# Kernel tuning notes

Measured on AMD Instinct MI355X. Metric: run time of the kernel, lower is better.

The kernel has to match this reference:

```python
import jax, jax.numpy as jnp
import numpy as np
from jax import lax

B, H, W = 32, 40, 256
FREQ = 40            # freq_num
WIND = 0.5           # wind_size (seconds)
KF = 5               # input_filter_kernel (odd -> 'same' length)
CNN_OUT = 64 * 36 * 252  # out_channels[-1] * (H-4) * (W-4)


def setup_inputs() -> dict:
    key = jax.random.key(0)
    ks = jax.random.split(key, 9)
    return {
        "inputs": jax.random.normal(ks[0], (B, 1, H, W), jnp.float32),
        "w0": jax.random.normal(ks[1], (32, 1, 3, 3), jnp.float32) * 0.1,
        "b0": jax.random.normal(ks[2], (32,), jnp.float32) * 0.05,
        "w1": jax.random.normal(ks[3], (64, 32, 3, 3), jnp.float32) * 0.05,
        "b1": jax.random.normal(ks[4], (64,), jnp.float32) * 0.05,
        "wf": jax.random.normal(ks[5], (1, 1, 1, KF), jnp.float32) * 0.2,
        "bf": jax.random.normal(ks[6], (1,), jnp.float32) * 0.05,
        "wr": jax.random.normal(ks[7], (FREQ, CNN_OUT), jnp.float32) * 1e-3,
        "br": jax.random.normal(ks[8], (FREQ,), jnp.float32) * 0.05,
    }


def _conv2d(x, w, padding):
    return lax.conv_general_dilated(
        x, w, window_strides=(1, 1), padding=padding,
        dimension_numbers=("NCHW", "OIHW", "NCHW"))


def reference(inputs, w0, b0, w1, b1, wf, bf, wr, br):
    b, _, h, w_len = inputs.shape
    # input_filter: Conv1d(1,1,KF, padding=KF//2) applied independently per
    # frequency row -> equivalent to a 2D conv with a (1,KF) kernel.
    p = KF // 2
    feats = _conv2d(inputs, wf, [(0, 0), (p, p)]) + bf[None, :, None, None]  # [B,1,H,W]

    # conv stack with ReLU
    x = jax.nn.relu(_conv2d(inputs, w0, "VALID") + b0[None, :, None, None])
    x = jax.nn.relu(_conv2d(x, w1, "VALID") + b1[None, :, None, None])

    gates = jax.nn.sigmoid(x.reshape(b, -1) @ wr.T + br)

    fs = (1.0 / WIND) * jnp.linspace(1.0, FREQ, FREQ)          # [FREQ]
    wtd_mean_mod = jnp.mean(gates * fs[None, :])               # scalar

    # Fused modulation transform: instead of the per-frequency python loop
    # with materialized [B,H,W] broadcasts, compute sin/cos bases [FREQ,W]
    # and reduce over time with a single einsum each.
    t = jnp.linspace(0.0, WIND, w_len)                          # [W]
    phase = (2.0 * np.pi) * fs[:, None] * t[None, :]            # [FREQ,W]
    f0 = feats[:, 0]                                            # [B,H,W]
    inv_w = jnp.float32(1.0 / w_len)
    sins = jnp.einsum("fw,bhw->bfh", jnp.sin(phase), f0) * inv_w  # mean over W
    coss = jnp.einsum("fw,bhw->bfh", jnp.cos(phase), f0) * inv_w
    mag = jnp.sqrt(sins * sins + coss * coss)                   # [B,FREQ,H]
    mods = (mag * gates[:, :, None]).reshape(b, FREQ * h)       # cat over freq, dim=1
    return mods, wtd_mean_mod
```

## Files before the change

kernel.cpp:

```cpp
#include <hip/hip_runtime.h>
#include <hip/hip_bf16.h>
#include <math.h>

#define BB   32
#define HH   40
#define WW   256
#define NF   40
#define H1N  36
#define W1N  252
#define KCNN 580608
#define KPW  192

typedef __attribute__((ext_vector_type(8))) short bf16x8;
typedef __attribute__((ext_vector_type(4))) float f32x4;

static __device__ __forceinline__ unsigned short f2bf(float v) {
    __hip_bfloat16 h = __float2bfloat16(v);
    return *(unsigned short*)&h;
}

static __device__ __forceinline__ bf16x8 packbf(float4 lo, float4 hi) {
    bf16x8 r;
    r[0] = (short)f2bf(lo.x); r[1] = (short)f2bf(lo.y);
    r[2] = (short)f2bf(lo.z); r[3] = (short)f2bf(lo.w);
    r[4] = (short)f2bf(hi.x); r[5] = (short)f2bf(hi.y);
    r[6] = (short)f2bf(hi.z); r[7] = (short)f2bf(hi.w);
    return r;
}

__global__ void k0_prep_w1(const float* __restrict__ w1, unsigned short* __restrict__ w1c,
                           float* __restrict__ gacc, float* __restrict__ out) {
    int o = blockIdx.x * 256 + threadIdx.x;
    int c0  = o & 31;
    int c1  = (o >> 5) & 63;
    int tap = o >> 11;
    w1c[o] = f2bf(w1[(c1 * 32 + c0) * 9 + tap]);
    if (blockIdx.x == 0) {
        for (int p = threadIdx.x; p < 1280; p += 256) gacc[p] = 0.0f;
        if (threadIdx.x == 0) out[51200] = 0.0f;
    }
}

__global__ __launch_bounds__(256) void k1_conv(
        const float* __restrict__ inp, const float* __restrict__ w0,
        const float* __restrict__ b0, const unsigned short* __restrict__ w1c,
        const float* __restrict__ b1, unsigned short* __restrict__ xbf) {
    __shared__ __align__(16) char smem[33856];
    float* ins = (float*)smem;
    unsigned short* y0T = (unsigned short*)(smem + 2176);
    unsigned short* stg = (unsigned short*)smem;

    const int jt = blockIdx.x;
    const int it = blockIdx.y;
    const int b  = blockIdx.z;
    const int i0 = it * 4;
    const int j0 = jt * 64;
    const int tid = threadIdx.x;

    for (int s = tid; s < 544; s += 256) {
        int r = s / 68, c = s - r * 68;
        int gc = j0 + c;
        ins[s] = (gc < WW) ? inp[(b * HH + i0 + r) * WW + gc] : 0.0f;
    }
    __syncthreads();

    {
        const int c0 = tid & 31;
        const int pg = tid >> 5;
        float wreg[9];
        #pragma unroll
        for (int k = 0; k < 9; ++k) wreg[k] = w0[c0 * 9 + k];
        const float bias = b0[c0];
        for (int it2 = 0; it2 < 50; ++it2) {
            int pos = it2 * 8 + pg;
            if (pos < 396) {
                int r   = pos / 66;
                int col = pos - r * 66;
                float v = 0.0f;
                if (j0 + col < 254) {
                    float a = bias;
                    #pragma unroll
                    for (int ki = 0; ki < 3; ++ki)
                        #pragma unroll
                        for (int kj = 0; kj < 3; ++kj)
                            a = fmaf(ins[(r + ki) * 68 + col + kj], wreg[ki * 3 + kj], a);
                    v = fmaxf(a, 0.0f);
                }
                y0T[pos * 40 + c0] = f2bf(v);
            }
        }
    }
    __syncthreads();

    const int w    = tid >> 6;
    const int lane = tid & 63;
    const int l15  = lane & 15;
    const int quad = lane >> 4;

    float biasr[4][4];
    #pragma unroll
    for (int mt = 0; mt < 4; ++mt)
        #pragma unroll
        for (int rg = 0; rg < 4; ++rg)
            biasr[mt][rg] = b1[mt * 16 + quad * 4 + rg];

    f32x4 acc[4][4];
    #pragma unroll
    for (int mt = 0; mt < 4; ++mt)
        #pragma unroll
        for (int nt = 0; nt < 4; ++nt)
            acc[mt][nt] = (f32x4){0.f, 0.f, 0.f, 0.f};

    #pragma unroll
    for (int ki = 0; ki < 3; ++ki) {
        #pragma unroll
        for (int kj = 0; kj < 3; ++kj) {
            const int tap = ki * 3 + kj;
            bf16x8 af[4], bfr[4];
            #pragma unroll
            for (int mt = 0; mt < 4; ++mt)
                af[mt] = *(const bf16x8*)(w1c + ((tap * 64 + mt * 16 + l15) * 32 + quad * 8));
            #pragma unroll
            for (int nt = 0; nt < 4; ++nt)
                bfr[nt] = *(const bf16x8*)(y0T + (((w + ki) * 66 + nt * 16 + l15 + kj) * 40 + quad * 8));
            #pragma unroll
            for (int mt = 0; mt < 4; ++mt)
                #pragma unroll
                for (int nt = 0; nt < 4; ++nt)
                    acc[mt][nt] = __builtin_amdgcn_mfma_f32_16x16x32_bf16(
                        af[mt], bfr[nt], acc[mt][nt], 0, 0, 0);
        }
    }

    __syncthreads();
    #pragma unroll
    for (int mt = 0; mt < 4; ++mt)
        #pragma unroll
        for (int nt = 0; nt < 4; ++nt)
            #pragma unroll
            for (int rg = 0; rg < 4; ++rg) {
                int c1 = mt * 16 + quad * 4 + rg;
                int j  = nt * 16 + l15;
                int jr = (j + (((c1 >> 2) & 3) << 4)) & 63;
                float v = fmaxf(acc[mt][nt][rg] + biasr[mt][rg], 0.0f);
                stg[(c1 * 4 + w) * 64 + jr] = f2bf(v);
            }
    __syncthreads();

    const int limit = (j0 + 64 <= W1N) ? 64 : (W1N - j0);
    for (int it2 = 0; it2 < 16; ++it2) {
        int cc = it2 * 256 + tid;
        int e  = cc * 4;
        int c1 = e >> 8;
        int w2 = (e >> 6) & 3;
        int jb = e & 63;
        if (jb < limit) {
            int jr = (jb + (((c1 >> 2) & 3) << 4)) & 63;
            *(uint2*)(xbf + (size_t)b * KCNN + (c1 * H1N + i0 + w2) * W1N + j0 + jb) =
                *(const uint2*)(stg + (c1 * 4 + w2) * 64 + jr);
        }
    }
}

__global__ __launch_bounds__(256) void k2_gemm(
        const unsigned short* __restrict__ xbf, const float* __restrict__ wr,
        float* __restrict__ gacc) {
    __shared__ float red[4][32][41];

    const int tid  = threadIdx.x;
    const int wv   = tid >> 6;
    const int lane = tid & 63;
    const int l15  = lane & 15;
    const int quad = lane >> 4;
    const size_t kw = (size_t)(blockIdx.x * 4 + wv) * KPW;

    const unsigned short* ap0 = xbf + (size_t)l15 * KCNN + kw + quad * 8;
    const unsigned short* ap1 = ap0 + (size_t)16 * KCNN;
    const float* bp0 = wr + (size_t)l15 * KCNN + kw + quad * 8;
    const float* bp1 = bp0 + (size_t)16 * KCNN;
    const bool v2 = (l15 < 8);
    const float* bp2 = bp0 + (size_t)32 * KCNN;

    f32x4 acc[2][3];
    #pragma unroll
    for (int mt = 0; mt < 2; ++mt)
        #pragma unroll
        for (int nt = 0; nt < 3; ++nt)
            acc[mt][nt] = (f32x4){0.f, 0.f, 0.f, 0.f};

    const float4 fz = {0.f, 0.f, 0.f, 0.f};
    bf16x8 a0c, a1c, a0n, a1n;
    float4 bw[3][2], bwn[3][2];

    a0c = *(const bf16x8*)ap0;
    a1c = *(const bf16x8*)ap1;
    bw[0][0] = *(const float4*)bp0; bw[0][1] = *(const float4*)(bp0 + 4);
    bw[1][0] = *(const float4*)bp1; bw[1][1] = *(const float4*)(bp1 + 4);
    if (v2) { bw[2][0] = *(const float4*)bp2; bw[2][1] = *(const float4*)(bp2 + 4); }
    else    { bw[2][0] = fz; bw[2][1] = fz; }

    for (int c = 0; c < 6; ++c) {
        if (c < 5) {
            const int o2 = (c + 1) * 32;
            a0n = *(const bf16x8*)(ap0 + o2);
            a1n = *(const bf16x8*)(ap1 + o2);
            bwn[0][0] = *(const float4*)(bp0 + o2); bwn[0][1] = *(const float4*)(bp0 + o2 + 4);
            bwn[1][0] = *(const float4*)(bp1 + o2); bwn[1][1] = *(const float4*)(bp1 + o2 + 4);
            if (v2) { bwn[2][0] = *(const float4*)(bp2 + o2); bwn[2][1] = *(const float4*)(bp2 + o2 + 4); }
            else    { bwn[2][0] = fz; bwn[2][1] = fz; }
        }
        #pragma unroll
        for (int nt = 0; nt < 3; ++nt) {
            bf16x8 bfrag = packbf(bw[nt][0], bw[nt][1]);
            acc[0][nt] = __builtin_amdgcn_mfma_f32_16x16x32_bf16(a0c, bfrag, acc[0][nt], 0, 0, 0);
            acc[1][nt] = __builtin_amdgcn_mfma_f32_16x16x32_bf16(a1c, bfrag, acc[1][nt], 0, 0, 0);
        }
        if (c < 5) {
            a0c = a0n; a1c = a1n;
            #pragma unroll
            for (int nt = 0; nt < 3; ++nt) { bw[nt][0] = bwn[nt][0]; bw[nt][1] = bwn[nt][1]; }
        }
    }

    #pragma unroll
    for (int mt = 0; mt < 2; ++mt)
        #pragma unroll
        for (int nt = 0; nt < 3; ++nt)
            #pragma unroll
            for (int rg = 0; rg < 4; ++rg) {
                int bb = mt * 16 + quad * 4 + rg;
                int ff = nt * 16 + l15;
                if (ff < NF) red[wv][bb][ff] = acc[mt][nt][rg];
            }
    __syncthreads();
    for (int p = tid; p < 1280; p += 256) {
        int bb = p / 40, ff = p - bb * 40;
        float s = 0.0f;
        #pragma unroll
        for (int w = 0; w < 4; ++w) s += red[w][bb][ff];
        atomicAdd(gacc + p, s);
    }
}

__global__ void k3_gates(const float* __restrict__ gacc, const float* __restrict__ br,
                         float* __restrict__ gates, float* __restrict__ out) {
    int p = blockIdx.x * 64 + threadIdx.x;
    int f = p % 40;
    float g = 1.0f / (1.0f + __expf(-(gacc[p] + br[f])));
    gates[p] = g;
    float c = g * (2.0f * (float)(f + 1)) * (1.0f / 1280.0f);
    #pragma unroll
    for (int off = 32; off >= 1; off >>= 1)
        c += __shfl_down(c, off, 64);
    if (threadIdx.x == 0) atomicAdd(out + 51200, c);
}

__global__ __launch_bounds__(320) void k4_mods(
        const float* __restrict__ inp, const float* __restrict__ wf,
        const float* __restrict__ bfp, const float* __restrict__ gates,
        float* __restrict__ out) {
    const int f = blockIdx.x, b = blockIdx.y;
    const int tid = threadIdx.x;
    const int h  = tid >> 3;
    const int wl = tid & 7;
    float wfv[5];
    #pragma unroll
    for (int t = 0; t < 5; ++t) wfv[t] = wf[t];
    const float bias = bfp[0];
    const float cph = 6.283185307179586f * (float)(f + 1) / 255.0f;
    const float* row = inp + (b * HH + h) * WW;
    float sa = 0.0f, ca = 0.0f;
    for (int m = 0; m < 32; ++m) {
        int w = wl + 8 * m;
        float feat = bias;
        #pragma unroll
        for (int d = -2; d <= 2; ++d) {
            int wc = w + d;
            if (wc >= 0 && wc < WW) feat = fmaf(row[wc], wfv[d + 2], feat);
        }
        float sv, cv;
        __sincosf(cph * (float)w, &sv, &cv);
        sa = fmaf(sv, feat, sa);
        ca = fmaf(cv, feat, ca);
    }
    #pragma unroll
    for (int off = 4; off >= 1; off >>= 1) {
        sa += __shfl_xor(sa, off, 8);
        ca += __shfl_xor(ca, off, 8);
    }
    if (wl == 0) {
        float mag = sqrtf(sa * sa + ca * ca) * (1.0f / 256.0f);
        out[b * 1600 + f * 40 + h] = mag * gates[b * 40 + f];
    }
}

extern "C" void kernel_launch(void* const* d_in, const int* in_sizes, int n_in,
                              void* d_out, int out_size, void* d_ws, size_t ws_size,
                              hipStream_t stream) {
    const float* inp = (const float*)d_in[0];
    const float* w0  = (const float*)d_in[1];
    const float* b0  = (const float*)d_in[2];
    const float* w1  = (const float*)d_in[3];
    const float* b1  = (const float*)d_in[4];
    const float* wf  = (const float*)d_in[5];
    const float* bf_ = (const float*)d_in[6];
    const float* wr  = (const float*)d_in[7];
    const float* br  = (const float*)d_in[8];
    float* out = (float*)d_out;

    char* ws = (char*)d_ws;
    unsigned short* xbf = (unsigned short*)ws;
    unsigned short* w1c = (unsigned short*)(ws + 37158912);
    float* gacc  = (float*)(ws + 37195776);
    float* gates = (float*)(ws + 37200896);

    k0_prep_w1<<<72, 256, 0, stream>>>(w1, w1c, gacc, out);
    k1_conv<<<dim3(4, 9, 32), 256, 0, stream>>>(inp, w0, b0, w1c, b1, xbf);
    k2_gemm<<<756, 256, 0, stream>>>(xbf, wr, gacc);
    k3_gates<<<20, 64, 0, stream>>>(gacc, br, gates, out);
    k4_mods<<<dim3(40, 32), 320, 0, stream>>>(inp, wf, bf_, gates, out);
}
```

Baseline: 225.8 us.

## Fuse gates into GEMM tail, tabulate sin/cos, register-block conv0, spread atomics

Several changes land together. The gates kernel is folded into the tail of the regression GEMM through a last-block counter, and the GEMM's atomic accumulation is spread across 8 replica buffers to cut contention. The sin/cos bases are precomputed into tables in the prep kernel and read by the modulation kernel. The first conv layer is restructured so each of 6 thread groups handles one output row using float4 register windows, replacing the strided per-position loop. Together these aim to remove a launch, reduce atomic serialization and trig cost, and cut LDS reads in conv0, at the cost of extra workspace and a threadfence/counter pattern.

```diff
diff --git a/kernel.cpp b/kernel.cpp
--- a/kernel.cpp
+++ b/kernel.cpp
@@ -10,6 +10,7 @@
 #define W1N  252
 #define KCNN 580608
 #define KPW  192
+#define NBLK2 756
 
 typedef __attribute__((ext_vector_type(8))) short bf16x8;
 typedef __attribute__((ext_vector_type(4))) float f32x4;
@@ -28,17 +29,23 @@
     return r;
 }
 
-__global__ void k0_prep_w1(const float* __restrict__ w1, unsigned short* __restrict__ w1c,
-                           float* __restrict__ gacc, float* __restrict__ out) {
+__global__ void k0_prep(const float* __restrict__ w1, unsigned short* __restrict__ w1c,
+                        float* __restrict__ gacc8, float* __restrict__ sintab,
+                        float* __restrict__ costab, float* __restrict__ out,
+                        int* __restrict__ cnt) {
     int o = blockIdx.x * 256 + threadIdx.x;
     int c0  = o & 31;
     int c1  = (o >> 5) & 63;
     int tap = o >> 11;
     w1c[o] = f2bf(w1[(c1 * 32 + c0) * 9 + tap]);
-    if (blockIdx.x == 0) {
-        for (int p = threadIdx.x; p < 1280; p += 256) gacc[p] = 0.0f;
-        if (threadIdx.x == 0) out[51200] = 0.0f;
-    }
+    if (o < 10240) {
+        int f = o >> 8, w = o & 255;
+        float ph = 6.283185307179586f * (float)(f + 1) * (1.0f / 255.0f) * (float)w;
+        sintab[o] = sinf(ph);
+        costab[o] = cosf(ph);
+        gacc8[o] = 0.0f;
+    }
+    if (o == 0) { out[51200] = 0.0f; cnt[0] = 0; }
 }
 
 __global__ __launch_bounds__(256) void k1_conv(
@@ -67,26 +74,56 @@
     {
         const int c0 = tid & 31;
         const int pg = tid >> 5;
-        float wreg[9];
-        #pragma unroll
-        for (int k = 0; k < 9; ++k) wreg[k] = w0[c0 * 9 + k];
-        const float bias = b0[c0];
-        for (int it2 = 0; it2 < 50; ++it2) {
-            int pos = it2 * 8 + pg;
-            if (pos < 396) {
-                int r   = pos / 66;
-                int col = pos - r * 66;
-                float v = 0.0f;
-                if (j0 + col < 254) {
+        if (pg < 6) {
+            float wreg[9];
+            #pragma unroll
+            for (int k = 0; k < 9; ++k) wreg[k] = w0[c0 * 9 + k];
+            const float bias = b0[c0];
+            const float4* rp0 = (const float4*)(ins + (pg    ) * 68);
+            const float4* rp1 = (const float4*)(ins + (pg + 1) * 68);
+            const float4* rp2 = (const float4*)(ins + (pg + 2) * 68);
+            unsigned short* yrow = y0T + pg * 66 * 40 + c0;
+            float4 a0 = rp0[0], a1 = rp1[0], a2 = rp2[0];
+            #pragma unroll 2
+            for (int ch = 0; ch < 8; ++ch) {
+                float4 b0v = rp0[2 * ch + 1], c0v = rp0[2 * ch + 2];
+                float4 b1v = rp1[2 * ch + 1], c1v = rp1[2 * ch + 2];
+                float4 b2v = rp2[2 * ch + 1], c2v = rp2[2 * ch + 2];
+                float r0[12] = {a0.x,a0.y,a0.z,a0.w,b0v.x,b0v.y,b0v.z,b0v.w,c0v.x,c0v.y,c0v.z,c0v.w};
+                float r1[12] = {a1.x,a1.y,a1.z,a1.w,b1v.x,b1v.y,b1v.z,b1v.w,c1v.x,c1v.y,c1v.z,c1v.w};
+                float r2[12] = {a2.x,a2.y,a2.z,a2.w,b2v.x,b2v.y,b2v.z,b2v.w,c2v.x,c2v.y,c2v.z,c2v.w};
+                #pragma unroll
+                for (int t = 0; t < 8; ++t) {
+                    int col = ch * 8 + t;
                     float a = bias;
                     #pragma unroll
-                    for (int ki = 0; ki < 3; ++ki)
-                        #pragma unroll
-                        for (int kj = 0; kj < 3; ++kj)
-                            a = fmaf(ins[(r + ki) * 68 + col + kj], wreg[ki * 3 + kj], a);
-                    v = fmaxf(a, 0.0f);
+                    for (int kj = 0; kj < 3; ++kj) {
+                        a = fmaf(r0[t + kj], wreg[kj],     a);
+                        a = fmaf(r1[t + kj], wreg[3 + kj], a);
+                        a = fmaf(r2[t + kj], wreg[6 + kj], a);
+                    }
+                    float v = (j0 + col < 254) ? fmaxf(a, 0.0f) : 0.0f;
+                    yrow[col * 40] = f2bf(v);
                 }
-                y0T[pos * 40 + c0] = f2bf(v);
+                a0 = c0v; a1 = c1v; a2 = c2v;
+            }
+            {
+                float t0[4] = {a0.x, a0.y, a0.z, a0.w};
+                float t1[4] = {a1.x, a1.y, a1.z, a1.w};
+                float t2[4] = {a2.x, a2.y, a2.z, a2.w};
+                #pragma unroll
+                for (int t = 0; t < 2; ++t) {
+                    int col = 64 + t;
+                    float a = bias;
+                    #pragma unroll
+                    for (int kj = 0; kj < 3; ++kj) {
+                        a = fmaf(t0[t + kj], wreg[kj],     a);
+                        a = fmaf(t1[t + kj], wreg[3 + kj], a);
+                        a = fmaf(t2[t + kj], wreg[6 + kj], a);
+                    }
+                    float v = (j0 + col < 254) ? fmaxf(a, 0.0f) : 0.0f;
+                    yrow[col * 40] = f2bf(v);
+                }
             }
         }
     }
@@ -164,8 +201,11 @@
 
 __global__ __launch_bounds__(256) void k2_gemm(
         const unsigned short* __restrict__ xbf, const float* __restrict__ wr,
-        float* __restrict__ gacc) {
+        float* __restrict__ gacc8, const float* __restrict__ br,
+        float* __restrict__ gates, float* __restrict__ out, int* __restrict__ cnt) {
     __shared__ float red[4][32][41];
+    __shared__ float wsum[4];
+    __shared__ int lastflag;
 
     const int tid  = threadIdx.x;
     const int wv   = tid >> 6;
@@ -233,30 +273,42 @@
                 if (ff < NF) red[wv][bb][ff] = acc[mt][nt][rg];
             }
     __syncthreads();
+    float* myg = gacc8 + (size_t)(blockIdx.x & 7) * 1280;
     for (int p = tid; p < 1280; p += 256) {
         int bb = p / 40, ff = p - bb * 40;
         float s = 0.0f;
         #pragma unroll
         for (int w = 0; w < 4; ++w) s += red[w][bb][ff];
-        atomicAdd(gacc + p, s);
-    }
-}
-
-__global__ void k3_gates(const float* __restrict__ gacc, const float* __restrict__ br,
-                         float* __restrict__ gates, float* __restrict__ out) {
-    int p = blockIdx.x * 64 + threadIdx.x;
-    int f = p % 40;
-    float g = 1.0f / (1.0f + __expf(-(gacc[p] + br[f])));
-    gates[p] = g;
-    float c = g * (2.0f * (float)(f + 1)) * (1.0f / 1280.0f);
-    #pragma unroll
-    for (int off = 32; off >= 1; off >>= 1)
-        c += __shfl_down(c, off, 64);
-    if (threadIdx.x == 0) atomicAdd(out + 51200, c);
+        atomicAdd(myg + p, s);
+    }
+
+    __threadfence();
+    __syncthreads();
+    if (tid == 0) lastflag = (atomicAdd(cnt, 1) == NBLK2 - 1) ? 1 : 0;
+    __syncthreads();
+    if (lastflag) {
+        float c = 0.0f;
+        for (int p = tid; p < 1280; p += 256) {
+            float s = 0.0f;
+            #pragma unroll
+            for (int r = 0; r < 8; ++r)
+                s += atomicAdd(gacc8 + r * 1280 + p, 0.0f);
+            int f = p % 40;
+            float g = 1.0f / (1.0f + __expf(-(s + br[f])));
+            gates[p] = g;
+            c += g * (2.0f * (float)(f + 1)) * (1.0f / 1280.0f);
+        }
+        #pragma unroll
+        for (int off = 32; off >= 1; off >>= 1) c += __shfl_down(c, off, 64);
+        if ((tid & 63) == 0) wsum[tid >> 6] = c;
+        __syncthreads();
+        if (tid == 0) out[51200] = wsum[0] + wsum[1] + wsum[2] + wsum[3];
+    }
 }
 
 __global__ __launch_bounds__(320) void k4_mods(
-        const float* __restrict__ inp, const float* __restrict__ wf,
+        const float* __restrict__ inp, const float* __restrict__ sintab,
+        const float* __restrict__ costab, const float* __restrict__ wf,
         const float* __restrict__ bfp, const float* __restrict__ gates,
         float* __restrict__ out) {
     const int f = blockIdx.x, b = blockIdx.y;
@@ -267,8 +319,9 @@
     #pragma unroll
     for (int t = 0; t < 5; ++t) wfv[t] = wf[t];
     const float bias = bfp[0];
-    const float cph = 6.283185307179586f * (float)(f + 1) / 255.0f;
-    const float* row = inp + (b * HH + h) * WW;
+    const float* row  = inp + (b * HH + h) * WW;
+    const float* srow = sintab + f * 256;
+    const float* crow = costab + f * 256;
     float sa = 0.0f, ca = 0.0f;
     for (int m = 0; m < 32; ++m) {
         int w = wl + 8 * m;
@@ -278,10 +331,8 @@
             int wc = w + d;
             if (wc >= 0 && wc < WW) feat = fmaf(row[wc], wfv[d + 2], feat);
         }
-        float sv, cv;
-        __sincosf(cph * (float)w, &sv, &cv);
-        sa = fmaf(sv, feat, sa);
-        ca = fmaf(cv, feat, ca);
+        sa = fmaf(srow[w], feat, sa);
+        ca = fmaf(crow[w], feat, ca);
     }
     #pragma unroll
     for (int off = 4; off >= 1; off >>= 1) {
@@ -311,12 +362,14 @@
     char* ws = (char*)d_ws;
     unsigned short* xbf = (unsigned short*)ws;
     unsigned short* w1c = (unsigned short*)(ws + 37158912);
-    float* gacc  = (float*)(ws + 37195776);
-    float* gates = (float*)(ws + 37200896);
-
-    k0_prep_w1<<<72, 256, 0, stream>>>(w1, w1c, gacc, out);
+    float* gacc8  = (float*)(ws + 37195776);
+    float* gates  = (float*)(ws + 37236736);
+    float* sintab = (float*)(ws + 37241856);
+    float* costab = (float*)(ws + 37282816);
+    int*   cnt    = (int*)(ws + 37323776);
+
+    k0_prep<<<72, 256, 0, stream>>>(w1, w1c, gacc8, sintab, costab, out, cnt);
     k1_conv<<<dim3(4, 9, 32), 256, 0, stream>>>(inp, w0, b0, w1c, b1, xbf);
-    k2_gemm<<<756, 256, 0, stream>>>(xbf, wr, gacc);
-    k3_gates<<<20, 64, 0, stream>>>(gacc, br, gates, out);
-    k4_mods<<<dim3(40, 32), 320, 0, stream>>>(inp, wf, bf_, gates, out);
-}
+    k2_gemm<<<756, 256, 0, stream>>>(xbf, wr, gacc8, br, gates, out, cnt);
+    k4_mods<<<dim3(40, 32), 320, 0, stream>>>(inp, sintab, costab, wf, bf_, gates, out);
+}
```

Measured after the change: 334.9 us. +48.3%, slower.
